# Kernel optimization log

Hardware: AMD Instinct MI355X
Metric: run time of the kernel (lower is better)

Reference implementation:

```python
import jax, jax.numpy as jnp
import numpy as np

DEPTH = 7  # leaves = 2**(DEPTH-1) = 64

def setup_inputs() -> dict:
    key = jax.random.key(0)
    k1, k2, k3 = jax.random.split(key, 3)
    bs, dimx, dimy = 32768, 2048, 2048
    leaves = 2 ** (DEPTH - 1)
    x = jax.random.normal(k1, (bs, dimx), dtype=jnp.float32)
    w = 0.1 * jax.random.uniform(k2, (dimx, leaves - 1), dtype=jnp.float32)
    b = jnp.zeros((leaves - 1,), dtype=jnp.float32)
    responses = 0.1 * jax.random.uniform(k3, (leaves, dimy), dtype=jnp.float32)
    return {"x": x, "w": w, "b": b, "responses": responses}

def reference(x, w, b, responses):
    bs = x.shape[0]
    # gate probabilities for all internal nodes of the binary tree: [bs, leaves-1]
    gate = jax.nn.sigmoid(x @ w + b)
    running = jnp.ones((bs, 1), dtype=x.dtype)
    for i in range(1, DEPTH):
        parents = gate[:, 2 ** (i - 1) - 1: 2 ** i - 1]  # [bs, 2**(i-1)]
        # torch.stack([left, right], dim=1).reshape -> [left | right] concat order
        running = jnp.concatenate([parents * running, (1.0 - parents) * running], axis=1)
    return running @ responses  # [bs, dimy]
```

## Files before the change

### kernel.cpp

```cpp
#include <hip/hip_runtime.h>
#include <hip/hip_bf16.h>


typedef short bf16x8 __attribute__((ext_vector_type(8)));
typedef float f32x4  __attribute__((ext_vector_type(4)));

#define BS    32768
#define DIMX  2048
#define NODES 63
#define NL    64
#define DIMY  2048

__device__ __forceinline__ unsigned short f2bf(float f) {
    union { float f; unsigned int u; } v; v.f = f;
    unsigned int r = v.u + 0x7FFFu + ((v.u >> 16) & 1u);
    return (unsigned short)(r >> 16);
}
__device__ __forceinline__ float bf2f(unsigned short h) {
    union { float f; unsigned int u; } v; v.u = ((unsigned int)h) << 16;
    return v.f;
}

__global__ __launch_bounds__(256) void prep(const float* __restrict__ w,
                                            const float* __restrict__ R,
                                            unsigned short* __restrict__ wFs,
                                            unsigned short* __restrict__ RTs) {
    int f = blockIdx.x * 256 + threadIdx.x;
    if (f < 262144) {
        int e   = f & 7;
        int l   = (f >> 3) & 63;
        int hl  = (f >> 9) & 1;
        int g16 = (f >> 10) & 3;
        int kk  = (f >> 12) & 1;
        int k   = f >> 13;
        int n    = g16 * 16 + (l & 15);
        int kcol = k * 64 + kk * 32 + (l >> 4) * 8 + e;
        float v = (n < NODES) ? w[(size_t)kcol * NODES + n] : 0.0f;
        unsigned short h = f2bf(v);
        wFs[f] = hl ? f2bf(v - bf2f(h)) : h;
    } else {
        int f2 = f - 262144;
        int e  = f2 & 7;
        int l  = (f2 >> 3) & 63;
        int kh = (f2 >> 9) & 1;
        int nf = f2 >> 10;
        int k  = kh * 32 + (l >> 4) * 8 + e;
        int n  = nf * 16 + (l & 15);
        RTs[f2] = f2bf(R[(size_t)k * DIMY + n]);
    }
}

#define GBM   16
#define GBK   64
#define GLD   72
#define NSTEP (DIMX / GBK)

__global__ __launch_bounds__(256, 8) void fused_kernel(const float* __restrict__ x,
                                                       const unsigned short* __restrict__ wFs,
                                                       const float* __restrict__ bias,
                                                       const unsigned short* __restrict__ RTs,
                                                       float* __restrict__ out) {
    __shared__ __align__(16) unsigned short xs[GBM][GLD];
    __shared__ float gl[GBM][NL + 1];

    const int t    = threadIdx.x;
    const int lane = t & 63;
    const int wv   = t >> 6;
    const int lr   = lane & 15;
    const int lg   = lane >> 4;
    const int m0   = blockIdx.x * GBM;

    const int xr = t >> 4;
    const int xc = (t & 15) * 4;
    const float* xsrc = x + (size_t)(m0 + xr) * DIMX + xc;

    const unsigned short* wb = wFs + (size_t)lane * 8;
    #define WFRAG(k, kk, hl) \
        (*(const bf16x8*)(wb + (size_t)((((k) * 2 + (kk)) * 4 + wv) * 2 + (hl)) * 512))

    float4 rx = *(const float4*)(xsrc);

    f32x4 acc = (f32x4){0.f, 0.f, 0.f, 0.f};

    for (int k = 0; k < NSTEP; ++k) {
        __syncthreads();
        {
            union { __hip_bfloat162 h2[2]; ushort4 v; } u;
            u.h2[0] = __float22bfloat162_rn(make_float2(rx.x, rx.y));
            u.h2[1] = __float22bfloat162_rn(make_float2(rx.z, rx.w));
            *(ushort4*)&xs[xr][xc] = u.v;
        }
        __syncthreads();
        if (k + 1 < NSTEP)
            rx = *(const float4*)(xsrc + (k + 1) * GBK);
        #pragma unroll
        for (int kk = 0; kk < 2; ++kk) {
            bf16x8 a = *(const bf16x8*)&xs[lr][kk * 32 + lg * 8];
            bf16x8 bh = WFRAG(k, kk, 0);
            bf16x8 bo = WFRAG(k, kk, 1);
            acc = __builtin_amdgcn_mfma_f32_16x16x32_bf16(a, bh, acc, 0, 0, 0);
            acc = __builtin_amdgcn_mfma_f32_16x16x32_bf16(a, bo, acc, 0, 0, 0);
        }
    }
    #undef WFRAG

    {
        const int col = wv * 16 + lr;
        const float bb = bias[col < NODES ? col : 0];
        #pragma unroll
        for (int i = 0; i < 4; ++i) {
            float s = acc[i] + bb;
            gl[lg * 4 + i][col] = 1.0f / (1.0f + __expf(-s));
        }
    }
    __syncthreads();

    {
        const int rr  = t >> 4;
        const int sub = t & 15;
        const int b5 = sub & 1, b4 = (sub >> 1) & 1, qq = sub >> 2;
        const float* g = gl[rr];
        float a2[2], a4[4], a8[8];
        float g0 = g[0];
        a2[0] = g0; a2[1] = 1.f - g0;
        #pragma unroll
        for (int m = 0; m < 4; ++m) {
            float gg = g[1 + (m & 1)];
            a4[m] = a2[m & 1] * ((m & 2) ? (1.f - gg) : gg);
        }
        #pragma unroll
        for (int m = 0; m < 8; ++m) {
            float gg = g[3 + (m & 3)];
            a8[m] = a4[m & 3] * ((m & 4) ? (1.f - gg) : gg);
        }
        unsigned short o[4];
        #pragma unroll
        for (int j = 0; j < 4; ++j) {
            int m = qq * 4 + j;
            float g4 = g[7 + (m & 7)];
            float p  = a8[m & 7] * ((m & 8) ? (1.f - g4) : g4);
            float g5 = g[15 + m];
            p *= b4 ? (1.f - g5) : g5;
            float g6 = g[31 + m + 16 * b4];
            p *= b5 ? (1.f - g6) : g6;
            o[j] = f2bf(p);
        }
        uint2 qv;
        qv.x = (unsigned)o[0] | ((unsigned)o[1] << 16);
        qv.y = (unsigned)o[2] | ((unsigned)o[3] << 16);
        *(uint2*)&xs[rr][b5 * 32 + b4 * 16 + qq * 4] = qv;
    }
    __syncthreads();

    bf16x8 pa[2];
    #pragma unroll
    for (int kh = 0; kh < 2; ++kh)
        pa[kh] = *(const bf16x8*)&xs[lr][kh * 32 + lg * 8];

    const unsigned short* bbase = RTs + (size_t)lane * 8;
    #define BLD(s, ci, kh) \
        (*(const bf16x8*)(bbase + (size_t)((((s) * 8 + wv * 2 + (ci)) * 2 + (kh))) * 512))

    float* op = out + (size_t)(m0 + lg * 4) * DIMY + wv * 32 + lr;

    #pragma unroll
    for (int s = 0; s < 16; ++s) {
        bf16x8 c00 = BLD(s, 0, 0), c01 = BLD(s, 0, 1);
        bf16x8 c10 = BLD(s, 1, 0), c11 = BLD(s, 1, 1);
        f32x4 oa0 = (f32x4){0.f, 0.f, 0.f, 0.f};
        f32x4 oa1 = (f32x4){0.f, 0.f, 0.f, 0.f};
        oa0 = __builtin_amdgcn_mfma_f32_16x16x32_bf16(pa[0], c00, oa0, 0, 0, 0);
        oa0 = __builtin_amdgcn_mfma_f32_16x16x32_bf16(pa[1], c01, oa0, 0, 0, 0);
        oa1 = __builtin_amdgcn_mfma_f32_16x16x32_bf16(pa[0], c10, oa1, 0, 0, 0);
        oa1 = __builtin_amdgcn_mfma_f32_16x16x32_bf16(pa[1], c11, oa1, 0, 0, 0);
        #pragma unroll
        for (int i = 0; i < 4; ++i) {
            op[(size_t)i * DIMY + s * 128]      = oa0[i];
            op[(size_t)i * DIMY + s * 128 + 16] = oa1[i];
        }
    }
    #undef BLD
}

extern "C" void kernel_launch(void* const* d_in, const int* in_sizes, int n_in,
                              void* d_out, int out_size, void* d_ws, size_t ws_size,
                              hipStream_t stream) {
    const float* x = (const float*)d_in[0];
    const float* w = (const float*)d_in[1];
    const float* b = (const float*)d_in[2];
    const float* R = (const float*)d_in[3];
    float* out = (float*)d_out;

    char* ws = (char*)d_ws;
    unsigned short* wFs = (unsigned short*)ws;
    unsigned short* RTs = (unsigned short*)(ws + 524288);

    prep<<<dim3(1536), 256, 0, stream>>>(w, R, wFs, RTs);
    fused_kernel<<<dim3(BS / GBM), 256, 0, stream>>>(x, wFs, b, RTs, out);
}
```

Measured before the change: 182.8 us.

## Split K across two waves with register-shuffled A fragments, dropping LDS staging

The block shrinks to 128 threads (two waves). The gate GEMM is split along K: each wave covers half of DIMX for all 64 node columns. Each wave loads x straight from global memory and rebuilds its MFMA A fragments with lane shuffles, so the per-step LDS round trip and the two barriers per K step are gone. Partial sums are reduced in LDS together with the bias before the sigmoid, and each wave then writes half of the output columns. The cost is more accumulator registers, redundant sigmoid evaluations in the tree stage, and half as many waves per block, which may reduce latency hiding on the memory-bound x read.

```diff
diff --git a/kernel.cpp b/kernel.cpp
--- a/kernel.cpp
+++ b/kernel.cpp
@@ -50,18 +50,16 @@
     }
 }
 
-#define GBM   16
-#define GBK   64
-#define GLD   72
-#define NSTEP (DIMX / GBK)
-
-__global__ __launch_bounds__(256, 8) void fused_kernel(const float* __restrict__ x,
+#define GBM 16
+
+__global__ __launch_bounds__(128, 4) void fused_kernel(const float* __restrict__ x,
                                                        const unsigned short* __restrict__ wFs,
                                                        const float* __restrict__ bias,
                                                        const unsigned short* __restrict__ RTs,
                                                        float* __restrict__ out) {
-    __shared__ __align__(16) unsigned short xs[GBM][GLD];
-    __shared__ float gl[GBM][NL + 1];
+    __shared__ float bl[NL];
+    __shared__ float glp[2][GBM][NL + 1];
+    __shared__ __align__(16) unsigned short pt[GBM][72];
 
     const int t    = threadIdx.x;
     const int lane = t & 63;
@@ -70,116 +68,127 @@
     const int lg   = lane >> 4;
     const int m0   = blockIdx.x * GBM;
 
-    const int xr = t >> 4;
-    const int xc = (t & 15) * 4;
-    const float* xsrc = x + (size_t)(m0 + xr) * DIMX + xc;
-
+    if (t < NL) bl[t] = (t < NODES) ? bias[t] : 0.0f;
+
+    const int xr = lane >> 2;
+    const int xc = lane & 3;
+    const float* xw = x + (size_t)(m0 + xr) * DIMX + xc * 8;
+    const int srcl = (lr << 2) | lg;
     const unsigned short* wb = wFs + (size_t)lane * 8;
-    #define WFRAG(k, kk, hl) \
-        (*(const bf16x8*)(wb + (size_t)((((k) * 2 + (kk)) * 4 + wv) * 2 + (hl)) * 512))
-
-    float4 rx = *(const float4*)(xsrc);
-
-    f32x4 acc = (f32x4){0.f, 0.f, 0.f, 0.f};
-
-    for (int k = 0; k < NSTEP; ++k) {
-        __syncthreads();
+
+    f32x4 acc[4];
+    #pragma unroll
+    for (int g = 0; g < 4; ++g) acc[g] = (f32x4){0.f, 0.f, 0.f, 0.f};
+
+    const int kbeg = wv * 16;
+    #pragma unroll 2
+    for (int ks = 0; ks < 16; ++ks) {
+        const int k = kbeg + ks;
+        const float* xk = xw + (size_t)k * 64;
+        float4 v0 = *(const float4*)(xk);
+        float4 v1 = *(const float4*)(xk + 4);
+        float4 v2 = *(const float4*)(xk + 32);
+        float4 v3 = *(const float4*)(xk + 36);
+        int q[8];
         {
-            union { __hip_bfloat162 h2[2]; ushort4 v; } u;
-            u.h2[0] = __float22bfloat162_rn(make_float2(rx.x, rx.y));
-            u.h2[1] = __float22bfloat162_rn(make_float2(rx.z, rx.w));
-            *(ushort4*)&xs[xr][xc] = u.v;
-        }
-        __syncthreads();
-        if (k + 1 < NSTEP)
-            rx = *(const float4*)(xsrc + (k + 1) * GBK);
-        #pragma unroll
-        for (int kk = 0; kk < 2; ++kk) {
-            bf16x8 a = *(const bf16x8*)&xs[lr][kk * 32 + lg * 8];
-            bf16x8 bh = WFRAG(k, kk, 0);
-            bf16x8 bo = WFRAG(k, kk, 1);
-            acc = __builtin_amdgcn_mfma_f32_16x16x32_bf16(a, bh, acc, 0, 0, 0);
-            acc = __builtin_amdgcn_mfma_f32_16x16x32_bf16(a, bo, acc, 0, 0, 0);
-        }
-    }
-    #undef WFRAG
+            union { __hip_bfloat162 h; int i; } u;
+            u.h = __float22bfloat162_rn(make_float2(v0.x, v0.y)); q[0] = u.i;
+            u.h = __float22bfloat162_rn(make_float2(v0.z, v0.w)); q[1] = u.i;
+            u.h = __float22bfloat162_rn(make_float2(v1.x, v1.y)); q[2] = u.i;
+            u.h = __float22bfloat162_rn(make_float2(v1.z, v1.w)); q[3] = u.i;
+            u.h = __float22bfloat162_rn(make_float2(v2.x, v2.y)); q[4] = u.i;
+            u.h = __float22bfloat162_rn(make_float2(v2.z, v2.w)); q[5] = u.i;
+            u.h = __float22bfloat162_rn(make_float2(v3.x, v3.y)); q[6] = u.i;
+            u.h = __float22bfloat162_rn(make_float2(v3.z, v3.w)); q[7] = u.i;
+        }
+        union { int i[4]; bf16x8 v; } A0, A1;
+        #pragma unroll
+        for (int j = 0; j < 4; ++j) {
+            A0.i[j] = __shfl(q[j], srcl);
+            A1.i[j] = __shfl(q[4 + j], srcl);
+        }
+        #pragma unroll
+        for (int g = 0; g < 4; ++g) {
+            const size_t b0 = (size_t)(((k * 2 + 0) * 4 + g) * 2) * 512;
+            const size_t b1 = (size_t)(((k * 2 + 1) * 4 + g) * 2) * 512;
+            bf16x8 bh0 = *(const bf16x8*)(wb + b0);
+            bf16x8 bo0 = *(const bf16x8*)(wb + b0 + 512);
+            bf16x8 bh1 = *(const bf16x8*)(wb + b1);
+            bf16x8 bo1 = *(const bf16x8*)(wb + b1 + 512);
+            acc[g] = __builtin_amdgcn_mfma_f32_16x16x32_bf16(A0.v, bh0, acc[g], 0, 0, 0);
+            acc[g] = __builtin_amdgcn_mfma_f32_16x16x32_bf16(A0.v, bo0, acc[g], 0, 0, 0);
+            acc[g] = __builtin_amdgcn_mfma_f32_16x16x32_bf16(A1.v, bh1, acc[g], 0, 0, 0);
+            acc[g] = __builtin_amdgcn_mfma_f32_16x16x32_bf16(A1.v, bo1, acc[g], 0, 0, 0);
+        }
+    }
+
+    #pragma unroll
+    for (int g = 0; g < 4; ++g)
+        #pragma unroll
+        for (int i = 0; i < 4; ++i)
+            glp[wv][lg * 4 + i][g * 16 + lr] = acc[g][i];
+    __syncthreads();
 
     {
-        const int col = wv * 16 + lr;
-        const float bb = bias[col < NODES ? col : 0];
-        #pragma unroll
-        for (int i = 0; i < 4; ++i) {
-            float s = acc[i] + bb;
-            gl[lg * 4 + i][col] = 1.0f / (1.0f + __expf(-s));
-        }
-    }
-    __syncthreads();
-
-    {
-        const int rr  = t >> 4;
-        const int sub = t & 15;
-        const int b5 = sub & 1, b4 = (sub >> 1) & 1, qq = sub >> 2;
-        const float* g = gl[rr];
+        const int rr  = wv * 8 + (lane >> 3);
+        const int sub = lane & 7;
+        const int b5 = sub & 1, b4 = (sub >> 1) & 1, mh = sub >> 2;
+        const float* p0 = glp[0][rr];
+        const float* p1 = glp[1][rr];
+        #define G(c) (1.0f / (1.0f + __expf(-(p0[c] + p1[c] + bl[c]))))
         float a2[2], a4[4], a8[8];
-        float g0 = g[0];
+        float g0 = G(0);
         a2[0] = g0; a2[1] = 1.f - g0;
         #pragma unroll
         for (int m = 0; m < 4; ++m) {
-            float gg = g[1 + (m & 1)];
+            float gg = G(1 + (m & 1));
             a4[m] = a2[m & 1] * ((m & 2) ? (1.f - gg) : gg);
         }
         #pragma unroll
         for (int m = 0; m < 8; ++m) {
-            float gg = g[3 + (m & 3)];
+            float gg = G(3 + (m & 3));
             a8[m] = a4[m & 3] * ((m & 4) ? (1.f - gg) : gg);
         }
-        unsigned short o[4];
-        #pragma unroll
-        for (int j = 0; j < 4; ++j) {
-            int m = qq * 4 + j;
-            float g4 = g[7 + (m & 7)];
+        unsigned short o[8];
+        #pragma unroll
+        for (int j = 0; j < 8; ++j) {
+            int m = mh * 8 + j;
+            float g4 = G(7 + (m & 7));
             float p  = a8[m & 7] * ((m & 8) ? (1.f - g4) : g4);
-            float g5 = g[15 + m];
+            float g5 = G(15 + m);
             p *= b4 ? (1.f - g5) : g5;
-            float g6 = g[31 + m + 16 * b4];
+            float g6 = G(31 + m + 16 * b4);
             p *= b5 ? (1.f - g6) : g6;
             o[j] = f2bf(p);
         }
-        uint2 qv;
-        qv.x = (unsigned)o[0] | ((unsigned)o[1] << 16);
-        qv.y = (unsigned)o[2] | ((unsigned)o[3] << 16);
-        *(uint2*)&xs[rr][b5 * 32 + b4 * 16 + qq * 4] = qv;
+        #undef G
+        uint4 q;
+        q.x = (unsigned)o[0] | ((unsigned)o[1] << 16);
+        q.y = (unsigned)o[2] | ((unsigned)o[3] << 16);
+        q.z = (unsigned)o[4] | ((unsigned)o[5] << 16);
+        q.w = (unsigned)o[6] | ((unsigned)o[7] << 16);
+        *(uint4*)&pt[rr][b5 * 32 + b4 * 16 + mh * 8] = q;
     }
     __syncthreads();
 
-    bf16x8 pa[2];
-    #pragma unroll
-    for (int kh = 0; kh < 2; ++kh)
-        pa[kh] = *(const bf16x8*)&xs[lr][kh * 32 + lg * 8];
-
-    const unsigned short* bbase = RTs + (size_t)lane * 8;
-    #define BLD(s, ci, kh) \
-        (*(const bf16x8*)(bbase + (size_t)((((s) * 8 + wv * 2 + (ci)) * 2 + (kh))) * 512))
-
-    float* op = out + (size_t)(m0 + lg * 4) * DIMY + wv * 32 + lr;
-
-    #pragma unroll
-    for (int s = 0; s < 16; ++s) {
-        bf16x8 c00 = BLD(s, 0, 0), c01 = BLD(s, 0, 1);
-        bf16x8 c10 = BLD(s, 1, 0), c11 = BLD(s, 1, 1);
-        f32x4 oa0 = (f32x4){0.f, 0.f, 0.f, 0.f};
-        f32x4 oa1 = (f32x4){0.f, 0.f, 0.f, 0.f};
-        oa0 = __builtin_amdgcn_mfma_f32_16x16x32_bf16(pa[0], c00, oa0, 0, 0, 0);
-        oa0 = __builtin_amdgcn_mfma_f32_16x16x32_bf16(pa[1], c01, oa0, 0, 0, 0);
-        oa1 = __builtin_amdgcn_mfma_f32_16x16x32_bf16(pa[0], c10, oa1, 0, 0, 0);
-        oa1 = __builtin_amdgcn_mfma_f32_16x16x32_bf16(pa[1], c11, oa1, 0, 0, 0);
-        #pragma unroll
-        for (int i = 0; i < 4; ++i) {
-            op[(size_t)i * DIMY + s * 128]      = oa0[i];
-            op[(size_t)i * DIMY + s * 128 + 16] = oa1[i];
-        }
-    }
-    #undef BLD
+    bf16x8 pa0 = *(const bf16x8*)&pt[lr][lg * 8];
+    bf16x8 pa1 = *(const bf16x8*)&pt[lr][32 + lg * 8];
+    const unsigned short* rb = RTs + (size_t)lane * 8;
+    float* op = out + (size_t)(m0 + lg * 4) * DIMY + lr;
+
+    const int nfb = wv * 64;
+    #pragma unroll 4
+    for (int s = 0; s < 64; ++s) {
+        const int nf = nfb + s;
+        bf16x8 c0 = *(const bf16x8*)(rb + (size_t)(nf * 2) * 512);
+        bf16x8 c1 = *(const bf16x8*)(rb + (size_t)(nf * 2 + 1) * 512);
+        f32x4 oa = (f32x4){0.f, 0.f, 0.f, 0.f};
+        oa = __builtin_amdgcn_mfma_f32_16x16x32_bf16(pa0, c0, oa, 0, 0, 0);
+        oa = __builtin_amdgcn_mfma_f32_16x16x32_bf16(pa1, c1, oa, 0, 0, 0);
+        #pragma unroll
+        for (int i = 0; i < 4; ++i)
+            op[(size_t)i * DIMY + nf * 16] = oa[i];
+    }
 }
 
 extern "C" void kernel_launch(void* const* d_in, const int* in_sizes, int n_in,
@@ -196,5 +205,5 @@
     unsigned short* RTs = (unsigned short*)(ws + 524288);
 
     prep<<<dim3(1536), 256, 0, stream>>>(w, R, wFs, RTs);
-    fused_kernel<<<dim3(BS / GBM), 256, 0, stream>>>(x, wFs, b, RTs, out);
-}
+    fused_kernel<<<dim3(BS / GBM), 128, 0, stream>>>(x, wFs, b, RTs, out);
+}
```

Result: faster. 161.0 us (-11.9%).

## Stage full x panel in LDS and split K across waves with reduction

Applied to the files above, without the earlier changes.

Each block now loads its whole 16x2048 x tile into a 64KB swizzled LDS panel with one bulk pass, instead of a 32-step loop with two barriers per step. Each wave then computes all 64 gate columns over its own quarter of K, and the four partial sums are reduced through LDS. The output GEMM gives each wave 32 contiguous column fragments. The large LDS footprint limits occupancy to about two blocks per CU, which trades latency hiding for fewer synchronisations and more independent MFMA chains.

```diff
diff --git a/kernel.cpp b/kernel.cpp
--- a/kernel.cpp
+++ b/kernel.cpp
@@ -50,68 +50,82 @@
     }
 }
 
-#define GBM   16
-#define GBK   64
-#define GLD   72
-#define NSTEP (DIMX / GBK)
-
-__global__ __launch_bounds__(256, 8) void fused_kernel(const float* __restrict__ x,
+#define FBM 16
+
+__global__ __launch_bounds__(256, 2) void fused_kernel(const float* __restrict__ x,
                                                        const unsigned short* __restrict__ wFs,
                                                        const float* __restrict__ bias,
                                                        const unsigned short* __restrict__ RTs,
                                                        float* __restrict__ out) {
-    __shared__ __align__(16) unsigned short xs[GBM][GLD];
-    __shared__ float gl[GBM][NL + 1];
+    __shared__ __align__(16) unsigned char smem[65536];
+    unsigned short* panel = (unsigned short*)smem;
+    float* glp = (float*)smem;
+    float* gl  = (float*)(smem + 17408);
+    unsigned short* pt = (unsigned short*)(smem + 22016);
 
     const int t    = threadIdx.x;
     const int lane = t & 63;
     const int wv   = t >> 6;
     const int lr   = lane & 15;
     const int lg   = lane >> 4;
-    const int m0   = blockIdx.x * GBM;
-
-    const int xr = t >> 4;
-    const int xc = (t & 15) * 4;
-    const float* xsrc = x + (size_t)(m0 + xr) * DIMX + xc;
-
-    const unsigned short* wb = wFs + (size_t)lane * 8;
-    #define WFRAG(k, kk, hl) \
-        (*(const bf16x8*)(wb + (size_t)((((k) * 2 + (kk)) * 4 + wv) * 2 + (hl)) * 512))
-
-    float4 rx = *(const float4*)(xsrc);
-
-    f32x4 acc = (f32x4){0.f, 0.f, 0.f, 0.f};
-
-    for (int k = 0; k < NSTEP; ++k) {
-        __syncthreads();
-        {
-            union { __hip_bfloat162 h2[2]; ushort4 v; } u;
-            u.h2[0] = __float22bfloat162_rn(make_float2(rx.x, rx.y));
-            u.h2[1] = __float22bfloat162_rn(make_float2(rx.z, rx.w));
-            *(ushort4*)&xs[xr][xc] = u.v;
-        }
-        __syncthreads();
-        if (k + 1 < NSTEP)
-            rx = *(const float4*)(xsrc + (k + 1) * GBK);
-        #pragma unroll
-        for (int kk = 0; kk < 2; ++kk) {
-            bf16x8 a = *(const bf16x8*)&xs[lr][kk * 32 + lg * 8];
-            bf16x8 bh = WFRAG(k, kk, 0);
-            bf16x8 bo = WFRAG(k, kk, 1);
-            acc = __builtin_amdgcn_mfma_f32_16x16x32_bf16(a, bh, acc, 0, 0, 0);
-            acc = __builtin_amdgcn_mfma_f32_16x16x32_bf16(a, bo, acc, 0, 0, 0);
-        }
-    }
-    #undef WFRAG
+    const int m0   = blockIdx.x * FBM;
 
     {
-        const int col = wv * 16 + lr;
-        const float bb = bias[col < NODES ? col : 0];
-        #pragma unroll
-        for (int i = 0; i < 4; ++i) {
-            float s = acc[i] + bb;
-            gl[lg * 4 + i][col] = 1.0f / (1.0f + __expf(-s));
-        }
+        const float* xsl = x + (size_t)m0 * DIMX;
+        #pragma unroll 8
+        for (int i = 0; i < 32; ++i) {
+            int o  = i * 1024 + t * 4;
+            float4 v = *(const float4*)(xsl + o);
+            int r  = o >> 11;
+            int k2 = (o & 2047) * 2;
+            union { __hip_bfloat162 h[2]; unsigned long long u; } u2;
+            u2.h[0] = __float22bfloat162_rn(make_float2(v.x, v.y));
+            u2.h[1] = __float22bfloat162_rn(make_float2(v.z, v.w));
+            *(unsigned long long*)((char*)panel + r * 4096 + (k2 ^ ((r & 7) << 4))) = u2.u;
+        }
+    }
+    __syncthreads();
+
+    f32x4 acc[4];
+    #pragma unroll
+    for (int g = 0; g < 4; ++g) acc[g] = (f32x4){0.f, 0.f, 0.f, 0.f};
+
+    {
+        const unsigned short* wb = wFs + (size_t)lane * 8;
+        const char* prow = (const char*)panel + lr * 4096;
+        #pragma unroll 4
+        for (int ks = 0; ks < 16; ++ks) {
+            const int k = wv * 512 + ks * 32;
+            const int colb = (k + lg * 8) * 2;
+            bf16x8 a = *(const bf16x8*)(prow + (colb ^ ((lr & 7) << 4)));
+            const size_t fb = (size_t)(k >> 5) * 8 * 512;
+            #pragma unroll
+            for (int g = 0; g < 4; ++g) {
+                const unsigned short* p = wb + fb + (size_t)g * 1024;
+                bf16x8 bh = *(const bf16x8*)p;
+                bf16x8 bo = *(const bf16x8*)(p + 512);
+                acc[g] = __builtin_amdgcn_mfma_f32_16x16x32_bf16(a, bh, acc[g], 0, 0, 0);
+                acc[g] = __builtin_amdgcn_mfma_f32_16x16x32_bf16(a, bo, acc[g], 0, 0, 0);
+            }
+        }
+    }
+    __syncthreads();
+
+    #pragma unroll
+    for (int g = 0; g < 4; ++g)
+        #pragma unroll
+        for (int i = 0; i < 4; ++i)
+            glp[wv * 1040 + (lg * 4 + i) * 65 + g * 16 + lr] = acc[g][i];
+    __syncthreads();
+
+    #pragma unroll
+    for (int ii = 0; ii < 4; ++ii) {
+        int j = t * 4 + ii;
+        int c = j & 63, r = j >> 6;
+        float s = glp[r * 65 + c] + glp[1040 + r * 65 + c]
+                + glp[2080 + r * 65 + c] + glp[3120 + r * 65 + c]
+                + ((c < NODES) ? bias[c] : 0.0f);
+        gl[r * 65 + c] = 1.0f / (1.0f + __expf(-s));
     }
     __syncthreads();
 
@@ -119,7 +133,7 @@
         const int rr  = t >> 4;
         const int sub = t & 15;
         const int b5 = sub & 1, b4 = (sub >> 1) & 1, qq = sub >> 2;
-        const float* g = gl[rr];
+        const float* g = gl + rr * 65;
         float a2[2], a4[4], a8[8];
         float g0 = g[0];
         a2[0] = g0; a2[1] = 1.f - g0;
@@ -148,38 +162,27 @@
         uint2 qv;
         qv.x = (unsigned)o[0] | ((unsigned)o[1] << 16);
         qv.y = (unsigned)o[2] | ((unsigned)o[3] << 16);
-        *(uint2*)&xs[rr][b5 * 32 + b4 * 16 + qq * 4] = qv;
-    }
-    __syncthreads();
-
-    bf16x8 pa[2];
-    #pragma unroll
-    for (int kh = 0; kh < 2; ++kh)
-        pa[kh] = *(const bf16x8*)&xs[lr][kh * 32 + lg * 8];
-
-    const unsigned short* bbase = RTs + (size_t)lane * 8;
-    #define BLD(s, ci, kh) \
-        (*(const bf16x8*)(bbase + (size_t)((((s) * 8 + wv * 2 + (ci)) * 2 + (kh))) * 512))
-
-    float* op = out + (size_t)(m0 + lg * 4) * DIMY + wv * 32 + lr;
-
-    #pragma unroll
-    for (int s = 0; s < 16; ++s) {
-        bf16x8 c00 = BLD(s, 0, 0), c01 = BLD(s, 0, 1);
-        bf16x8 c10 = BLD(s, 1, 0), c11 = BLD(s, 1, 1);
-        f32x4 oa0 = (f32x4){0.f, 0.f, 0.f, 0.f};
-        f32x4 oa1 = (f32x4){0.f, 0.f, 0.f, 0.f};
-        oa0 = __builtin_amdgcn_mfma_f32_16x16x32_bf16(pa[0], c00, oa0, 0, 0, 0);
-        oa0 = __builtin_amdgcn_mfma_f32_16x16x32_bf16(pa[1], c01, oa0, 0, 0, 0);
-        oa1 = __builtin_amdgcn_mfma_f32_16x16x32_bf16(pa[0], c10, oa1, 0, 0, 0);
-        oa1 = __builtin_amdgcn_mfma_f32_16x16x32_bf16(pa[1], c11, oa1, 0, 0, 0);
-        #pragma unroll
-        for (int i = 0; i < 4; ++i) {
-            op[(size_t)i * DIMY + s * 128]      = oa0[i];
-            op[(size_t)i * DIMY + s * 128 + 16] = oa1[i];
-        }
-    }
-    #undef BLD
+        *(uint2*)&pt[rr * 72 + b5 * 32 + b4 * 16 + qq * 4] = qv;
+    }
+    __syncthreads();
+
+    bf16x8 pa0 = *(const bf16x8*)&pt[lr * 72 + lg * 8];
+    bf16x8 pa1 = *(const bf16x8*)&pt[lr * 72 + 32 + lg * 8];
+    const unsigned short* rb = RTs + (size_t)lane * 8;
+    float* op = out + (size_t)(m0 + lg * 4) * DIMY + lr;
+
+    #pragma unroll 4
+    for (int s = 0; s < 32; ++s) {
+        const int nf = wv * 32 + s;
+        bf16x8 c0 = *(const bf16x8*)(rb + (size_t)(nf * 2) * 512);
+        bf16x8 c1 = *(const bf16x8*)(rb + (size_t)(nf * 2 + 1) * 512);
+        f32x4 oa = (f32x4){0.f, 0.f, 0.f, 0.f};
+        oa = __builtin_amdgcn_mfma_f32_16x16x32_bf16(pa0, c0, oa, 0, 0, 0);
+        oa = __builtin_amdgcn_mfma_f32_16x16x32_bf16(pa1, c1, oa, 0, 0, 0);
+        #pragma unroll
+        for (int i = 0; i < 4; ++i)
+            op[(size_t)i * DIMY + nf * 16] = oa[i];
+    }
 }
 
 extern "C" void kernel_launch(void* const* d_in, const int* in_sizes, int n_in,
@@ -196,5 +199,5 @@
     unsigned short* RTs = (unsigned short*)(ws + 524288);
 
     prep<<<dim3(1536), 256, 0, stream>>>(w, R, wFs, RTs);
-    fused_kernel<<<dim3(BS / GBM), 256, 0, stream>>>(x, wFs, b, RTs, out);
-}
+    fused_kernel<<<dim3(BS / FBM), 256, 0, stream>>>(x, wFs, b, RTs, out);
+}
```

After: 183.6 us. Within noise of the previous version (+0.5%).
